# Optimization experiments

Measured on AMD Instinct MI355X. Metric: run time of the kernel, lower is better.

Reference implementation:

```python
import jax, jax.numpy as jnp
import numpy as np

N = 1024      # num_nodes
U = 64        # num_units
IN_DIM = 2    # input feature dim per node
B = 32        # batch
F = IN_DIM + U  # 66, input_size inside _gconv


def _xavier(k, shape):
    fan_in, fan_out = shape[-2], shape[-1]
    std = (2.0 / (fan_in + fan_out)) ** 0.5
    return jax.random.normal(k, shape, jnp.float32) * std


def setup_inputs() -> dict:
    key = jax.random.key(0)
    ks = jax.random.split(key, 14)
    return {
        "inputs": jax.random.normal(ks[0], (B, N * IN_DIM), jnp.float32),
        "hx": jax.random.normal(ks[1], (B, N * U), jnp.float32),
        "adj": jax.random.uniform(ks[2], (2, N, N), jnp.float32),
        "mask": jax.random.uniform(ks[3], (8, N, N), jnp.float32),
        # gate gconv params (output_size = 2U). Note: torch LayerParams caches by
        # shape, so weights_s/weights_i/weights_bp are ONE shared weight, ditto atts/atti.
        "W_ru": _xavier(ks[4], (F, 2 * U)),
        "Watt_ru": _xavier(ks[5], (N, 2 * U, 2 * U)),
        "Watt1_ru": _xavier(ks[6], (N, 2 * U, 1)),
        "Wout_ru": _xavier(ks[7], (6 * U, 2 * U)),
        "b_ru": jnp.ones((2 * U,), jnp.float32),   # bias_start=1.0
        # candidate gconv params (output_size = U)
        "W_c": _xavier(ks[8], (F, U)),
        "Watt_c": _xavier(ks[9], (N, U, U)),
        "Watt1_c": _xavier(ks[10], (N, U, 1)),
        "Wout_c": _xavier(ks[11], (3 * U, U)),
        "b_c": jnp.zeros((U,), jnp.float32),
    }


def _gconv(inputs, state, adj, mask, W, Watt, Watt1, Wout, b):
    Bs = inputs.shape[0]
    x = jnp.concatenate([inputs.reshape(Bs, N, -1), state.reshape(Bs, N, -1)], axis=2)  # [B,N,F]
    Ff = x.shape[2]
    x0 = x.transpose(1, 2, 0).reshape(N, Ff * Bs)  # [N, F*B]
    a0, a1 = adj[0], adj[1]
    # supports in the exact order of the torch loop:
    # adj0, mask0..3*adj0, mask4..7*adj1, adj1  -> 10 matrices
    mats = jnp.concatenate(
        [a0[None], mask[:4] * a0[None], mask[4:] * a1[None], a1[None]], axis=0
    )  # [10,N,N]
    xk = jnp.einsum('mij,jf->mif', mats, x0)  # [10,N,F*B]
    x_all = jnp.concatenate([x0[None], xk], axis=0).reshape(11, N, Ff, Bs)
    x_bp = x_all[0].transpose(2, 0, 1)        # [B,N,F]
    x_i = x_all[1:6].transpose(3, 1, 0, 2)    # [B,N,5,F]
    x_s = x_all[6:].transpose(3, 1, 0, 2)     # [B,N,5,F]
    x_i_p = x_i @ W        # [B,N,5,O] (shared weight, see LayerParams shape cache)
    x_s_p = x_s @ W        # [B,N,5,O]
    x_bp_p = x_bp @ W      # [B,N,O]

    def attend(xp):
        h = jax.nn.relu(jnp.einsum('bnko,noq->bnkq', xp, Watt))     # per-node weights
        s = jnp.einsum('bnkq,nqo->bnko', h, Watt1)[..., 0]          # [B,N,5]
        a = jax.nn.softmax(s, axis=-1)                              # over 5 supports
        return jnp.einsum('bnk,bnko->bno', a, xp)                   # [B,N,O]

    xi = attend(x_i_p)
    xs = attend(x_s_p)
    out = jnp.concatenate([xi, xs, x_bp_p], axis=-1) @ Wout + b     # [B,N,O]
    return out.reshape(Bs, -1)


def reference(inputs, hx, adj, mask, W_ru, Watt_ru, Watt1_ru, Wout_ru, b_ru,
              W_c, Watt_c, Watt1_c, Wout_c, b_c):
    value = jax.nn.sigmoid(_gconv(inputs, hx, adj, mask, W_ru, Watt_ru, Watt1_ru, Wout_ru, b_ru))
    value = value.reshape(-1, N, 2 * U)
    r = value[..., :U].reshape(-1, N * U)
    u = value[..., U:].reshape(-1, N * U)
    c = jnp.tanh(_gconv(inputs, r * hx, adj, mask, W_c, Watt_c, Watt1_c, Wout_c, b_c))
    return u * hx + (1.0 - u) * c
```

## Files before the change

kernel.cpp:

```cpp
#include <hip/hip_runtime.h>
#include <hip/hip_fp16.h>
#include <cstdint>
#include <cstddef>

#define NN 1024
#define BB 32

typedef _Float16 f16x8 __attribute__((ext_vector_type(8)));
typedef _Float16 f16x4 __attribute__((ext_vector_type(4)));
typedef float f32x4 __attribute__((ext_vector_type(4)));

__device__ __forceinline__ void load_lds16(const void* g, void* l) {
  __builtin_amdgcn_global_load_lds(
      (const __attribute__((address_space(1))) void*)g,
      (__attribute__((address_space(3))) void*)l, 16, 0, 0);
}

__global__ __launch_bounds__(256) void k_build_amats(
    const float* __restrict__ adj, const float* __restrict__ mask,
    _Float16* __restrict__ A) {
  int q = blockIdx.x * 256 + threadIdx.x;
  int i = q >> 8;
  int j0 = (q & 255) << 2;
  size_t off = (size_t)i * 1024 + j0;
  float4 a0 = *(const float4*)(adj + off);
  float4 a1 = *(const float4*)(adj + (1u << 20) + off);
  f16x4 r;
  r[0] = a0.x; r[1] = a0.y; r[2] = a0.z; r[3] = a0.w;
  *(f16x4*)(A + off) = r;
  r[0] = a1.x; r[1] = a1.y; r[2] = a1.z; r[3] = a1.w;
  *(f16x4*)(A + (size_t)9 * 1048576 + off) = r;
#pragma unroll
  for (int l = 0; l < 8; ++l) {
    float4 mk = *(const float4*)(mask + (size_t)l * 1048576 + off);
    float4 base = (l < 4) ? a0 : a1;
    r[0] = mk.x * base.x; r[1] = mk.y * base.y;
    r[2] = mk.z * base.z; r[3] = mk.w * base.w;
    *(f16x4*)(A + (size_t)(l + 1) * 1048576 + off) = r;
  }
}

__global__ __launch_bounds__(256) void k_prep_wout(
    const float* __restrict__ Wru, const float* __restrict__ Wc,
    _Float16* __restrict__ WThru, _Float16* __restrict__ WTlru,
    _Float16* __restrict__ WThc, _Float16* __restrict__ WTlc) {
  int id = blockIdx.x * 256 + threadIdx.x;
  if (id < 128 * 384) {
    int o = id & 127, k = id >> 7;
    float w = Wru[k * 128 + o];
    _Float16 h = (_Float16)w;
    WThru[o * 384 + k] = h;
    WTlru[o * 384 + k] = (_Float16)(w - (float)h);
  } else {
    int id2 = id - 128 * 384;
    if (id2 < 64 * 192) {
      int o = id2 & 63, k = id2 >> 6;
      float w = Wc[k * 64 + o];
      _Float16 h = (_Float16)w;
      WThc[o * 192 + k] = h;
      WTlc[o * 192 + k] = (_Float16)(w - (float)h);
    }
  }
}

__global__ __launch_bounds__(256) void k_build_x0p(
    const float* __restrict__ inp, const float* __restrict__ state,
    _Float16* __restrict__ X0P) {
  const int b = blockIdx.x;
  const int j0 = blockIdx.y * 64;
  const int tid = threadIdx.x;
  for (int p = tid; p < 4096; p += 256) {
    int jj = p >> 6, f = p & 63;
    X0P[((size_t)(b * 1024 + j0 + jj)) * 96 + 2 + f] =
        (_Float16)state[(size_t)b * 65536 + (j0 + jj) * 64 + f];
  }
  if (tid < 128) {
    int jj = tid >> 1, f = tid & 1;
    X0P[((size_t)(b * 1024 + j0 + jj)) * 96 + f] =
        (_Float16)inp[(size_t)b * 2048 + (j0 + jj) * 2 + f];
    X0P[((size_t)(b * 1024 + j0 + 32 + jj)) * 96 + f] =
        (_Float16)inp[(size_t)b * 2048 + (j0 + 32 + jj) * 2 + f];
  }
  for (int p = tid; p < 64 * 32; p += 256) {
    int jj = p >> 5, f = 66 + (p & 31);
    if (f < 96)
      X0P[((size_t)(b * 1024 + j0 + jj)) * 96 + f] = (_Float16)0.f;
  }
}

template <int O>
__global__ __launch_bounds__(256, 2) void k_proj0_mfma(
    const _Float16* __restrict__ X0P, const float* __restrict__ W,
    _Float16* __restrict__ XP0, _Float16* __restrict__ XP0T) {
  constexpr int WR = O / 64;
  constexpr int WC = 4 / WR;
  constexpr int TN = WC * 64;
  constexpr int NPT = TN / 64;
  __shared__ _Float16 ldsB[2][TN * 32];
  const int tid = threadIdx.x;
  const int c0 = blockIdx.x * TN;
  const int b = c0 >> 10;
  const int l = tid & 63;
  const int w = tid >> 6;
  const int wr = w / WC, wc = w % WC;

  f16x8 af[4][3];
#pragma unroll
  for (int i = 0; i < 4; ++i) {
    int o = wr * 64 + i * 16 + (l & 15);
#pragma unroll
    for (int ks = 0; ks < 3; ++ks) {
#pragma unroll
      for (int e = 0; e < 8; ++e) {
        int f = ks * 32 + (l >> 4) * 8 + e;
        af[i][ks][e] = (f < 66) ? (_Float16)W[f * O + o] : (_Float16)0.f;
      }
    }
  }

  int tt[NPT], rr[NPT], qq[NPT];
#pragma unroll
  for (int u = 0; u < NPT; ++u) {
    tt[u] = u * 256 + tid;
    rr[u] = tt[u] >> 2;
    qq[u] = (tt[u] & 3) ^ (rr[u] & 3);
  }

  const int ps = ((l >> 4) ^ (l & 3)) * 8;
  int offB[4];
#pragma unroll
  for (int j = 0; j < 4; ++j)
    offB[j] = (wc * 64 + j * 16 + (l & 15)) * 32 + ps;

  f32x4 acc[4][4];
#pragma unroll
  for (int i = 0; i < 4; ++i)
#pragma unroll
    for (int j = 0; j < 4; ++j) acc[i][j] = (f32x4){0.f, 0.f, 0.f, 0.f};

#pragma unroll
  for (int u = 0; u < NPT; ++u)
    load_lds16(X0P + (size_t)(c0 + rr[u]) * 96 + qq[u] * 8,
               &ldsB[0][0] + tt[u] * 8);

  int buf = 0;
  for (int kt = 0; kt < 3; ++kt) {
    __syncthreads();
    if (kt + 1 < 3) {
#pragma unroll
      for (int u = 0; u < NPT; ++u)
        load_lds16(X0P + (size_t)(c0 + rr[u]) * 96 + (kt + 1) * 32 + qq[u] * 8,
                   &ldsB[buf ^ 1][0] + tt[u] * 8);
    }
    f16x8 bf[4];
#pragma unroll
    for (int j = 0; j < 4; ++j) bf[j] = *(const f16x8*)(&ldsB[buf][offB[j]]);
#pragma unroll
    for (int i = 0; i < 4; ++i)
#pragma unroll
      for (int j = 0; j < 4; ++j)
        acc[i][j] = __builtin_amdgcn_mfma_f32_16x16x32_f16(af[i][kt], bf[j],
                                                           acc[i][j], 0, 0, 0);
    buf ^= 1;
  }

#pragma unroll
  for (int i = 0; i < 4; ++i) {
    int ob = wr * 64 + i * 16 + (l >> 4) * 4;
#pragma unroll
    for (int j = 0; j < 4; ++j) {
      int jn = (c0 & 1023) + wc * 64 + j * 16 + (l & 15);
      f16x4 hv;
#pragma unroll
      for (int r = 0; r < 4; ++r) {
        hv[r] = (_Float16)acc[i][j][r];
        XP0T[((size_t)b * O + ob + r) * 1024 + jn] = hv[r];
      }
      *(f16x4*)(XP0 + ((size_t)jn * 32 + b) * O + ob) = hv;
    }
  }
}

template <int CN>
__global__ __launch_bounds__(256, 2) void k_supports2_mfma(
    const _Float16* __restrict__ A, const _Float16* __restrict__ BT,
    _Float16* __restrict__ XPD) {
  __shared__ _Float16 ldsA[2][4096];
  __shared__ _Float16 ldsB[2][4096];
  const int tid = threadIdx.x;
  const int bn = blockIdx.x;
  const int bm = blockIdx.y;
  const int l = tid & 63;
  const int w = tid >> 6;
  const int wr = w >> 1, wc = w & 1;

  const int t0 = tid, t1 = 256 + tid;
  const int r0 = t0 >> 2, q0 = (t0 & 3) ^ (r0 & 3);
  const int r1 = t1 >> 2, q1 = (t1 & 3) ^ (r1 & 3);
  const _Float16* gA0 = A + ((size_t)(bm * 128 + r0)) * 1024 + q0 * 8;
  const _Float16* gA1 = A + ((size_t)(bm * 128 + r1)) * 1024 + q1 * 8;
  const _Float16* gB0 = BT + ((size_t)(bn * 128 + r0)) * 1024 + q0 * 8;
  const _Float16* gB1 = BT + ((size_t)(bn * 128 + r1)) * 1024 + q1 * 8;

  const int ps = ((l >> 4) ^ (l & 3)) * 8;
  int offA[4], offB[4];
#pragma unroll
  for (int i = 0; i < 4; ++i) {
    offA[i] = (wr * 64 + i * 16 + (l & 15)) * 32 + ps;
    offB[i] = (wc * 64 + i * 16 + (l & 15)) * 32 + ps;
  }

  f32x4 acc[4][4];
#pragma unroll
  for (int i = 0; i < 4; ++i)
#pragma unroll
    for (int j = 0; j < 4; ++j) acc[i][j] = (f32x4){0.f, 0.f, 0.f, 0.f};

  load_lds16(gA0, &ldsA[0][0] + t0 * 8);
  load_lds16(gA1, &ldsA[0][0] + t1 * 8);
  load_lds16(gB0, &ldsB[0][0] + t0 * 8);
  load_lds16(gB1, &ldsB[0][0] + t1 * 8);

  int buf = 0;
  for (int kt = 0; kt < 32; ++kt) {
    __syncthreads();
    if (kt + 1 < 32) {
      int k0 = (kt + 1) * 32;
      load_lds16(gA0 + k0, &ldsA[buf ^ 1][0] + t0 * 8);
      load_lds16(gA1 + k0, &ldsA[buf ^ 1][0] + t1 * 8);
      load_lds16(gB0 + k0, &ldsB[buf ^ 1][0] + t0 * 8);
      load_lds16(gB1 + k0, &ldsB[buf ^ 1][0] + t1 * 8);
    }
    f16x8 af[4], bf[4];
#pragma unroll
    for (int i = 0; i < 4; ++i)
      af[i] = *(const f16x8*)(&ldsA[buf][offA[i]]);
#pragma unroll
    for (int i = 0; i < 4; ++i)
      bf[i] = *(const f16x8*)(&ldsB[buf][offB[i]]);
#pragma unroll
    for (int i = 0; i < 4; ++i)
#pragma unroll
      for (int j = 0; j < 4; ++j)
        acc[i][j] = __builtin_amdgcn_mfma_f32_16x16x32_f16(af[i], bf[j],
                                                           acc[i][j], 0, 0, 0);
    buf ^= 1;
  }

#pragma unroll
  for (int i = 0; i < 4; ++i) {
    int R = bm * 128 + wr * 64 + i * 16 + (l >> 4) * 4;
#pragma unroll
    for (int j = 0; j < 4; ++j) {
      int col = bn * 128 + wc * 64 + j * 16 + (l & 15);
#pragma unroll
      for (int r = 0; r < 4; ++r)
        XPD[(size_t)(R + r) * CN + col] = (_Float16)acc[i][j][r];
    }
  }
}

template <int O>
__global__ __launch_bounds__(256) void k_attend_mfma(
    const __half* __restrict__ XPD, const float* __restrict__ Watt,
    const float* __restrict__ Watt1, _Float16* __restrict__ CAT2h,
    _Float16* __restrict__ CAT2l) {
  constexpr int MTW = O / 64;
  constexpr int KS = O / 32;
  constexpr int SLOTS = O / 8;
  constexpr int SWZ = SLOTS - 1;
  constexpr int OH = O / 2;
  const int n = blockIdx.x;
  const int tid = threadIdx.x;
  const int l = tid & 63;
  const int w = tid >> 6;

  __shared__ _Float16 xpL[160 * O];
  __shared__ float sPartL[4][160];
  __shared__ float aL[32][5];

  const int qbase = w * (O / 4);
  f16x8 afr[MTW][KS];
#pragma unroll
  for (int mt = 0; mt < MTW; ++mt) {
    const int q = qbase + mt * 16 + (l & 15);
#pragma unroll
    for (int ks = 0; ks < KS; ++ks) {
#pragma unroll
      for (int e = 0; e < 8; ++e) {
        int o = ks * 32 + (l >> 4) * 8 + e;
        afr[mt][ks][e] = (_Float16)Watt[((size_t)n * O + o) * O + q];
      }
    }
  }
  float wt1[MTW][4];
#pragma unroll
  for (int mt = 0; mt < MTW; ++mt)
#pragma unroll
    for (int r = 0; r < 4; ++r)
      wt1[mt][r] = Watt1[(size_t)n * O + qbase + mt * 16 + (l >> 4) * 4 + r];

  for (int g = 0; g < 2; ++g) {
    if (g) __syncthreads();
    {
      const uint32_t* xsrc = reinterpret_cast<const uint32_t*>(XPD);
      uint32_t* xdst = reinterpret_cast<uint32_t*>(xpL);
      for (int p = tid; p < 160 * OH; p += 256) {
        int row = p / OH;
        int oh = p - row * OH;
        int slot = oh >> 2;
        int phys = slot ^ (row & SWZ);
        int si = row >> 5, b = row & 31;
        size_t gi = ((size_t)(g * 5 + si) * 1024 + n) * (size_t)(16 * O) +
                    b * OH + oh;
        xdst[row * OH + phys * 4 + (oh & 3)] = xsrc[gi];
      }
    }
    __syncthreads();

    for (int nt = 0; nt < 10; ++nt) {
      f32x4 acc[MTW];
#pragma unroll
      for (int mt = 0; mt < MTW; ++mt) acc[mt] = (f32x4){0.f, 0.f, 0.f, 0.f};
      const int row = nt * 16 + (l & 15);
#pragma unroll
      for (int ks = 0; ks < KS; ++ks) {
        int phys = (ks * 4 + (l >> 4)) ^ (row & SWZ);
        f16x8 bf = *(const f16x8*)(&xpL[row * O + phys * 8]);
#pragma unroll
        for (int mt = 0; mt < MTW; ++mt)
          acc[mt] = __builtin_amdgcn_mfma_f32_16x16x32_f16(afr[mt][ks], bf,
                                                           acc[mt], 0, 0, 0);
      }
      float sp = 0.f;
#pragma unroll
      for (int mt = 0; mt < MTW; ++mt)
#pragma unroll
        for (int r = 0; r < 4; ++r)
          sp += fmaxf(acc[mt][r], 0.f) * wt1[mt][r];
      sp += __shfl_xor(sp, 16);
      sp += __shfl_xor(sp, 32);
      if (l < 16) sPartL[w][nt * 16 + l] = sp;
    }
    __syncthreads();

    if (tid < 32) {
      const int b = tid;
      float sv[5];
#pragma unroll
      for (int k = 0; k < 5; ++k) {
        int row = k * 32 + b;
        sv[k] = sPartL[0][row] + sPartL[1][row] + sPartL[2][row] +
                sPartL[3][row];
      }
      float mx = sv[0];
#pragma unroll
      for (int k = 1; k < 5; ++k) mx = fmaxf(mx, sv[k]);
      float e[5], sum = 0.f;
#pragma unroll
      for (int k = 0; k < 5; ++k) {
        e[k] = expf(sv[k] - mx);
        sum += e[k];
      }
      float inv = 1.f / sum;
#pragma unroll
      for (int k = 0; k < 5; ++k) aL[b][k] = e[k] * inv;
    }
    __syncthreads();

    for (int it = 0; it < SLOTS * 32 / 256; ++it) {
      int idx = it * 256 + tid;
      int b = idx & 31;
      int sc = idx >> 5;
      float o8[8] = {0.f, 0.f, 0.f, 0.f, 0.f, 0.f, 0.f, 0.f};
#pragma unroll
      for (int si = 0; si < 5; ++si) {
        int row = si * 32 + b;
        int phys = sc ^ (row & SWZ);
        f16x8 xv = *(const f16x8*)(&xpL[row * O + phys * 8]);
        float a = aL[b][si];
#pragma unroll
        for (int j = 0; j < 8; ++j) o8[j] += a * (float)xv[j];
      }
      f16x8 hv, lv;
#pragma unroll
      for (int j = 0; j < 8; ++j) {
        hv[j] = (_Float16)o8[j];
        lv[j] = (_Float16)(o8[j] - (float)hv[j]);
      }
      size_t doff = ((size_t)n * 32 + b) * (2 * O) + g * O + sc * 8;
      *reinterpret_cast<f16x8*>(CAT2h + doff) = hv;
      *reinterpret_cast<f16x8*>(CAT2l + doff) = lv;
    }
  }
}

__global__ __launch_bounds__(256, 2) void k_wout_ru_mfma(
    const _Float16* __restrict__ CAT2h, const _Float16* __restrict__ CAT2l,
    const _Float16* __restrict__ XP0, const _Float16* __restrict__ WTh,
    const _Float16* __restrict__ WTl, const float* __restrict__ bias,
    const float* __restrict__ hx, float* __restrict__ RHX,
    float* __restrict__ UBUF) {
  constexpr int KTOT = 384, KC = 8, KT = 12;
  __shared__ _Float16 ldsAh[2][4096];
  __shared__ _Float16 ldsAl[2][4096];
  __shared__ _Float16 ldsBh[2][4096];
  __shared__ _Float16 ldsBl[2][4096];
  const int tid = threadIdx.x;
  const int blk = blockIdx.x;
  const int l = tid & 63;
  const int w = tid >> 6;
  const int wr = w >> 1, wc = w & 1;

  const int t0 = tid, t1 = 256 + tid;
  const int r0 = t0 >> 2, q0 = (t0 & 3) ^ (r0 & 3);
  const int r1 = t1 >> 2, q1 = (t1 & 3) ^ (r1 & 3);
  const size_t R0 = (size_t)blk * 128 + r0, R1 = (size_t)blk * 128 + r1;
  const _Float16* pA0ch = CAT2h + R0 * 256 + q0 * 8;
  const _Float16* pA1ch = CAT2h + R1 * 256 + q1 * 8;
  const _Float16* pA0cl = CAT2l + R0 * 256 + q0 * 8;
  const _Float16* pA1cl = CAT2l + R1 * 256 + q1 * 8;
  const _Float16* pA0x = XP0 + R0 * 128 + q0 * 8;
  const _Float16* pA1x = XP0 + R1 * 128 + q1 * 8;
  const _Float16* pB0h = WTh + (size_t)r0 * KTOT + q0 * 8;
  const _Float16* pB1h = WTh + (size_t)r1 * KTOT + q1 * 8;
  const _Float16* pB0l = WTl + (size_t)r0 * KTOT + q0 * 8;
  const _Float16* pB1l = WTl + (size_t)r1 * KTOT + q1 * 8;

  const int ps = ((l >> 4) ^ (l & 3)) * 8;
  int offA[4], offB[4];
#pragma unroll
  for (int i = 0; i < 4; ++i) {
    offA[i] = (wr * 64 + i * 16 + (l & 15)) * 32 + ps;
    offB[i] = (wc * 64 + i * 16 + (l & 15)) * 32 + ps;
  }

  f32x4 acc[4][4];
#pragma unroll
  for (int i = 0; i < 4; ++i)
#pragma unroll
    for (int j = 0; j < 4; ++j) acc[i][j] = (f32x4){0.f, 0.f, 0.f, 0.f};

  load_lds16(pA0ch, &ldsAh[0][0] + t0 * 8);
  load_lds16(pA1ch, &ldsAh[0][0] + t1 * 8);
  load_lds16(pA0cl, &ldsAl[0][0] + t0 * 8);
  load_lds16(pA1cl, &ldsAl[0][0] + t1 * 8);
  load_lds16(pB0h, &ldsBh[0][0] + t0 * 8);
  load_lds16(pB1h, &ldsBh[0][0] + t1 * 8);
  load_lds16(pB0l, &ldsBl[0][0] + t0 * 8);
  load_lds16(pB1l, &ldsBl[0][0] + t1 * 8);

  int buf = 0;
  for (int kt = 0; kt < KT; ++kt) {
    __syncthreads();
    if (kt + 1 < KT) {
      int k1 = kt + 1;
      const _Float16* a0 =
          (k1 < KC) ? pA0ch + k1 * 32 : pA0x + (k1 - KC) * 32;
      const _Float16* a1 =
          (k1 < KC) ? pA1ch + k1 * 32 : pA1x + (k1 - KC) * 32;
      load_lds16(a0, &ldsAh[buf ^ 1][0] + t0 * 8);
      load_lds16(a1, &ldsAh[buf ^ 1][0] + t1 * 8);
      if (k1 < KC) {
        load_lds16(pA0cl + k1 * 32, &ldsAl[buf ^ 1][0] + t0 * 8);
        load_lds16(pA1cl + k1 * 32, &ldsAl[buf ^ 1][0] + t1 * 8);
      }
      load_lds16(pB0h + k1 * 32, &ldsBh[buf ^ 1][0] + t0 * 8);
      load_lds16(pB1h + k1 * 32, &ldsBh[buf ^ 1][0] + t1 * 8);
      load_lds16(pB0l + k1 * 32, &ldsBl[buf ^ 1][0] + t0 * 8);
      load_lds16(pB1l + k1 * 32, &ldsBl[buf ^ 1][0] + t1 * 8);
    }
    f16x8 ah[4], bh[4], bl[4];
#pragma unroll
    for (int i = 0; i < 4; ++i) ah[i] = *(const f16x8*)(&ldsAh[buf][offA[i]]);
#pragma unroll
    for (int i = 0; i < 4; ++i) bh[i] = *(const f16x8*)(&ldsBh[buf][offB[i]]);
#pragma unroll
    for (int i = 0; i < 4; ++i) bl[i] = *(const f16x8*)(&ldsBl[buf][offB[i]]);
#pragma unroll
    for (int i = 0; i < 4; ++i)
#pragma unroll
      for (int j = 0; j < 4; ++j) {
        acc[i][j] = __builtin_amdgcn_mfma_f32_16x16x32_f16(ah[i], bh[j],
                                                           acc[i][j], 0, 0, 0);
        acc[i][j] = __builtin_amdgcn_mfma_f32_16x16x32_f16(ah[i], bl[j],
                                                           acc[i][j], 0, 0, 0);
      }
    if (kt < KC) {
      f16x8 al[4];
#pragma unroll
      for (int i = 0; i < 4; ++i)
        al[i] = *(const f16x8*)(&ldsAl[buf][offA[i]]);
#pragma unroll
      for (int i = 0; i < 4; ++i)
#pragma unroll
        for (int j = 0; j < 4; ++j)
          acc[i][j] = __builtin_amdgcn_mfma_f32_16x16x32_f16(al[i], bh[j],
                                                             acc[i][j], 0, 0, 0);
    }
    buf ^= 1;
  }

#pragma unroll
  for (int i = 0; i < 4; ++i) {
    int R = blk * 128 + wr * 64 + i * 16 + (l >> 4) * 4;
#pragma unroll
    for (int j = 0; j < 4; ++j) {
      int o = wc * 64 + j * 16 + (l & 15);
      float bv = bias[o];
#pragma unroll
      for (int rr = 0; rr < 4; ++rr) {
        int Rr = R + rr;
        int n = Rr >> 5, b = Rr & 31;
        size_t base = ((size_t)b * NN + n) * 64;
        float val = 1.f / (1.f + expf(-(acc[i][j][rr] + bv)));
        if (o < 64)
          RHX[base + o] = val * hx[base + o];
        else
          UBUF[base + (o - 64)] = val;
      }
    }
  }
}

__global__ __launch_bounds__(256, 2) void k_wout_c_mfma(
    const _Float16* __restrict__ CAT2h, const _Float16* __restrict__ CAT2l,
    const _Float16* __restrict__ XP0, const _Float16* __restrict__ WTh,
    const _Float16* __restrict__ WTl, const float* __restrict__ bias,
    const float* __restrict__ UBUF, const float* __restrict__ hx,
    float* __restrict__ out) {
  constexpr int KTOT = 192, KC = 4, KT = 6;
  __shared__ _Float16 ldsAh[2][4096];
  __shared__ _Float16 ldsAl[2][4096];
  __shared__ _Float16 ldsBh[2][2048];
  __shared__ _Float16 ldsBl[2][2048];
  const int tid = threadIdx.x;
  const int blk = blockIdx.x;
  const int l = tid & 63;
  const int w = tid >> 6;

  const int t0 = tid, t1 = 256 + tid;
  const int r0 = t0 >> 2, q0 = (t0 & 3) ^ (r0 & 3);
  const int r1 = t1 >> 2, q1 = (t1 & 3) ^ (r1 & 3);
  const size_t R0 = (size_t)blk * 128 + r0, R1 = (size_t)blk * 128 + r1;
  const _Float16* pA0ch = CAT2h + R0 * 128 + q0 * 8;
  const _Float16* pA1ch = CAT2h + R1 * 128 + q1 * 8;
  const _Float16* pA0cl = CAT2l + R0 * 128 + q0 * 8;
  const _Float16* pA1cl = CAT2l + R1 * 128 + q1 * 8;
  const _Float16* pA0x = XP0 + R0 * 64 + q0 * 8;
  const _Float16* pA1x = XP0 + R1 * 64 + q1 * 8;
  const int rb = tid >> 2, qb = (tid & 3) ^ (rb & 3);
  const _Float16* pBh = WTh + (size_t)rb * KTOT + qb * 8;
  const _Float16* pBl = WTl + (size_t)rb * KTOT + qb * 8;

  const int ps = ((l >> 4) ^ (l & 3)) * 8;
  int offA[2], offB[4];
#pragma unroll
  for (int i = 0; i < 2; ++i)
    offA[i] = (w * 32 + i * 16 + (l & 15)) * 32 + ps;
#pragma unroll
  for (int j = 0; j < 4; ++j) offB[j] = (j * 16 + (l & 15)) * 32 + ps;

  f32x4 acc[2][4];
#pragma unroll
  for (int i = 0; i < 2; ++i)
#pragma unroll
    for (int j = 0; j < 4; ++j) acc[i][j] = (f32x4){0.f, 0.f, 0.f, 0.f};

  load_lds16(pA0ch, &ldsAh[0][0] + t0 * 8);
  load_lds16(pA1ch, &ldsAh[0][0] + t1 * 8);
  load_lds16(pA0cl, &ldsAl[0][0] + t0 * 8);
  load_lds16(pA1cl, &ldsAl[0][0] + t1 * 8);
  load_lds16(pBh, &ldsBh[0][0] + tid * 8);
  load_lds16(pBl, &ldsBl[0][0] + tid * 8);

  int buf = 0;
  for (int kt = 0; kt < KT; ++kt) {
    __syncthreads();
    if (kt + 1 < KT) {
      int k1 = kt + 1;
      const _Float16* a0 =
          (k1 < KC) ? pA0ch + k1 * 32 : pA0x + (k1 - KC) * 32;
      const _Float16* a1 =
          (k1 < KC) ? pA1ch + k1 * 32 : pA1x + (k1 - KC) * 32;
      load_lds16(a0, &ldsAh[buf ^ 1][0] + t0 * 8);
      load_lds16(a1, &ldsAh[buf ^ 1][0] + t1 * 8);
      if (k1 < KC) {
        load_lds16(pA0cl + k1 * 32, &ldsAl[buf ^ 1][0] + t0 * 8);
        load_lds16(pA1cl + k1 * 32, &ldsAl[buf ^ 1][0] + t1 * 8);
      }
      load_lds16(pBh + k1 * 32, &ldsBh[buf ^ 1][0] + tid * 8);
      load_lds16(pBl + k1 * 32, &ldsBl[buf ^ 1][0] + tid * 8);
    }
    f16x8 ah[2], bh[4], bl[4];
#pragma unroll
    for (int i = 0; i < 2; ++i) ah[i] = *(const f16x8*)(&ldsAh[buf][offA[i]]);
#pragma unroll
    for (int j = 0; j < 4; ++j) bh[j] = *(const f16x8*)(&ldsBh[buf][offB[j]]);
#pragma unroll
    for (int j = 0; j < 4; ++j) bl[j] = *(const f16x8*)(&ldsBl[buf][offB[j]]);
#pragma unroll
    for (int i = 0; i < 2; ++i)
#pragma unroll
      for (int j = 0; j < 4; ++j) {
        acc[i][j] = __builtin_amdgcn_mfma_f32_16x16x32_f16(ah[i], bh[j],
                                                           acc[i][j], 0, 0, 0);
        acc[i][j] = __builtin_amdgcn_mfma_f32_16x16x32_f16(ah[i], bl[j],
                                                           acc[i][j], 0, 0, 0);
      }
    if (kt < KC) {
      f16x8 al[2];
#pragma unroll
      for (int i = 0; i < 2; ++i)
        al[i] = *(const f16x8*)(&ldsAl[buf][offA[i]]);
#pragma unroll
      for (int i = 0; i < 2; ++i)
#pragma unroll
        for (int j = 0; j < 4; ++j)
          acc[i][j] = __builtin_amdgcn_mfma_f32_16x16x32_f16(al[i], bh[j],
                                                             acc[i][j], 0, 0, 0);
    }
    buf ^= 1;
  }

#pragma unroll
  for (int i = 0; i < 2; ++i) {
    int R = blk * 128 + w * 32 + i * 16 + (l >> 4) * 4;
#pragma unroll
    for (int j = 0; j < 4; ++j) {
      int o = j * 16 + (l & 15);
      float bv = bias[o];
#pragma unroll
      for (int rr = 0; rr < 4; ++rr) {
        int Rr = R + rr;
        int n = Rr >> 5, b = Rr & 31;
        size_t idx = ((size_t)b * NN + n) * 64 + o;
        float cval = tanhf(acc[i][j][rr] + bv);
        float u = UBUF[idx];
        out[idx] = u * hx[idx] + (1.f - u) * cval;
      }
    }
  }
}

extern "C" void kernel_launch(void* const* d_in, const int* in_sizes, int n_in,
                              void* d_out, int out_size, void* d_ws,
                              size_t ws_size, hipStream_t stream) {
  const float* inputs   = (const float*)d_in[0];
  const float* hx       = (const float*)d_in[1];
  const float* adj      = (const float*)d_in[2];
  const float* mask     = (const float*)d_in[3];
  const float* W_ru     = (const float*)d_in[4];
  const float* Watt_ru  = (const float*)d_in[5];
  const float* Watt1_ru = (const float*)d_in[6];
  const float* Wout_ru  = (const float*)d_in[7];
  const float* b_ru     = (const float*)d_in[8];
  const float* W_c      = (const float*)d_in[9];
  const float* Watt_c   = (const float*)d_in[10];
  const float* Watt1_c  = (const float*)d_in[11];
  const float* Wout_c   = (const float*)d_in[12];
  const float* b_c      = (const float*)d_in[13];

  char* ws = (char*)d_ws;
  _Float16*  X0P   = (_Float16*)(ws);
  _Float16*  XPD   = (_Float16*)(ws + 6291456);
  _Float16*  XP0   = (_Float16*)(ws + 90177536);
  _Float16*  XP0T  = (_Float16*)(ws + 98566144);
  _Float16*  CAT2h = (_Float16*)(ws + 106954752);
  _Float16*  CAT2l = (_Float16*)(ws + 123731968);
  float*     RHX   = (float*)(ws + 140509184);
  float*     UBUF  = (float*)(ws + 148897792);
  _Float16*  A_all = (_Float16*)(ws + 157286400);
  _Float16*  WThru = (_Float16*)(ws + 178257920);
  _Float16*  WTlru = (_Float16*)(ws + 178356224);
  _Float16*  WThc  = (_Float16*)(ws + 178454528);
  _Float16*  WTlc  = (_Float16*)(ws + 178479104);
  float*     out   = (float*)d_out;

  k_build_amats<<<1024, 256, 0, stream>>>(adj, mask, A_all);
  k_prep_wout<<<240, 256, 0, stream>>>(Wout_ru, Wout_c, WThru, WTlru, WThc,
                                       WTlc);

  k_build_x0p<<<dim3(32, 16), 256, 0, stream>>>(inputs, hx, X0P);
  k_proj0_mfma<128><<<256, 256, 0, stream>>>(X0P, W_ru, XP0, XP0T);
  k_supports2_mfma<4096><<<dim3(32, 80), 256, 0, stream>>>(A_all, XP0T, XPD);
  k_attend_mfma<128><<<1024, 256, 0, stream>>>((const __half*)XPD, Watt_ru,
                                               Watt1_ru, CAT2h, CAT2l);
  k_wout_ru_mfma<<<256, 256, 0, stream>>>(CAT2h, CAT2l, XP0, WThru, WTlru,
                                          b_ru, hx, RHX, UBUF);
  k_build_x0p<<<dim3(32, 16), 256, 0, stream>>>(inputs, RHX, X0P);
  k_proj0_mfma<64><<<128, 256, 0, stream>>>(X0P, W_c, XP0, XP0T);
  k_supports2_mfma<2048><<<dim3(16, 80), 256, 0, stream>>>(A_all, XP0T, XPD);
  k_attend_mfma<64><<<1024, 256, 0, stream>>>((const __half*)XPD, Watt_c,
                                              Watt1_c, CAT2h, CAT2l);
  k_wout_c_mfma<<<256, 256, 0, stream>>>(CAT2h, CAT2l, XP0, WThc, WTlc, b_c,
                                         UBUF, hx, out);
}
```

Baseline: 344.5 us.

## Use 32x32 MFMA and XCD-aware block swizzle in supports GEMM; drop split-fp16 in wout_c

The supports GEMM switches from 16x16x32 MFMA tiles to 32x32x16 MFMA tiles. Fewer LDS fragment reads and MFMA issues are needed per K step. Workgroups are remapped so consecutive blocks on each XCD share A/B tiles in L2. Separately, the candidate Wout GEMM drops the low-order fp16 correction terms (hi/lo split), which removes extra loads and MFMAs at the cost of reduced precision in the final output.

Measured after the change: 374.6 us. 1.09x slower.

```diff
diff --git a/kernel.cpp b/kernel.cpp
--- a/kernel.cpp
+++ b/kernel.cpp
@@ -9,6 +9,7 @@
 typedef _Float16 f16x8 __attribute__((ext_vector_type(8)));
 typedef _Float16 f16x4 __attribute__((ext_vector_type(4)));
 typedef float f32x4 __attribute__((ext_vector_type(4)));
+typedef float f32x16 __attribute__((ext_vector_type(16)));
 
 __device__ __forceinline__ void load_lds16(const void* g, void* l) {
   __builtin_amdgcn_global_load_lds(
@@ -188,8 +189,13 @@
   __shared__ _Float16 ldsA[2][4096];
   __shared__ _Float16 ldsB[2][4096];
   const int tid = threadIdx.x;
-  const int bn = blockIdx.x;
-  const int bm = blockIdx.y;
+  constexpr int GX = CN / 128;
+  const int flat = blockIdx.x + GX * blockIdx.y;
+  constexpr int NWG = GX * 80;
+  constexpr int CPX = NWG / 8;
+  const int swz = (flat & 7) * CPX + (flat >> 3);
+  const int bn = swz % GX;
+  const int bm = swz / GX;
   const int l = tid & 63;
   const int w = tid >> 6;
   const int wr = w >> 1, wc = w & 1;
@@ -202,19 +208,23 @@
   const _Float16* gB0 = BT + ((size_t)(bn * 128 + r0)) * 1024 + q0 * 8;
   const _Float16* gB1 = BT + ((size_t)(bn * 128 + r1)) * 1024 + q1 * 8;
 
-  const int ps = ((l >> 4) ^ (l & 3)) * 8;
-  int offA[4], offB[4];
-#pragma unroll
-  for (int i = 0; i < 4; ++i) {
-    offA[i] = (wr * 64 + i * 16 + (l & 15)) * 32 + ps;
-    offB[i] = (wc * 64 + i * 16 + (l & 15)) * 32 + ps;
-  }
-
-  f32x4 acc[4][4];
-#pragma unroll
-  for (int i = 0; i < 4; ++i)
-#pragma unroll
-    for (int j = 0; j < 4; ++j) acc[i][j] = (f32x4){0.f, 0.f, 0.f, 0.f};
+  int offA[2][2], offB[2][2];
+#pragma unroll
+  for (int fi = 0; fi < 2; ++fi)
+#pragma unroll
+    for (int ks = 0; ks < 2; ++ks) {
+      int slot = ((ks * 2 + (l >> 5)) ^ (l & 3)) * 8;
+      offA[fi][ks] = (wr * 64 + fi * 32 + (l & 31)) * 32 + slot;
+      offB[fi][ks] = (wc * 64 + fi * 32 + (l & 31)) * 32 + slot;
+    }
+
+  f32x16 acc[2][2];
+#pragma unroll
+  for (int i = 0; i < 2; ++i)
+#pragma unroll
+    for (int j = 0; j < 2; ++j)
+#pragma unroll
+      for (int e = 0; e < 16; ++e) acc[i][j][e] = 0.f;
 
   load_lds16(gA0, &ldsA[0][0] + t0 * 8);
   load_lds16(gA1, &ldsA[0][0] + t1 * 8);
@@ -231,33 +241,37 @@
       load_lds16(gB0 + k0, &ldsB[buf ^ 1][0] + t0 * 8);
       load_lds16(gB1 + k0, &ldsB[buf ^ 1][0] + t1 * 8);
     }
-    f16x8 af[4], bf[4];
-#pragma unroll
-    for (int i = 0; i < 4; ++i)
-      af[i] = *(const f16x8*)(&ldsA[buf][offA[i]]);
-#pragma unroll
-    for (int i = 0; i < 4; ++i)
-      bf[i] = *(const f16x8*)(&ldsB[buf][offB[i]]);
-#pragma unroll
-    for (int i = 0; i < 4; ++i)
-#pragma unroll
-      for (int j = 0; j < 4; ++j)
-        acc[i][j] = __builtin_amdgcn_mfma_f32_16x16x32_f16(af[i], bf[j],
-                                                           acc[i][j], 0, 0, 0);
+    f16x8 af[2][2], bf[2][2];
+#pragma unroll
+    for (int fi = 0; fi < 2; ++fi)
+#pragma unroll
+      for (int ks = 0; ks < 2; ++ks) {
+        af[fi][ks] = *(const f16x8*)(&ldsA[buf][offA[fi][ks]]);
+        bf[fi][ks] = *(const f16x8*)(&ldsB[buf][offB[fi][ks]]);
+      }
+#pragma unroll
+    for (int fi = 0; fi < 2; ++fi)
+#pragma unroll
+      for (int fj = 0; fj < 2; ++fj)
+#pragma unroll
+        for (int ks = 0; ks < 2; ++ks)
+          acc[fi][fj] = __builtin_amdgcn_mfma_f32_32x32x16_f16(
+              af[fi][ks], bf[fj][ks], acc[fi][fj], 0, 0, 0);
     buf ^= 1;
   }
 
 #pragma unroll
-  for (int i = 0; i < 4; ++i) {
-    int R = bm * 128 + wr * 64 + i * 16 + (l >> 4) * 4;
-#pragma unroll
-    for (int j = 0; j < 4; ++j) {
-      int col = bn * 128 + wc * 64 + j * 16 + (l & 15);
-#pragma unroll
-      for (int r = 0; r < 4; ++r)
-        XPD[(size_t)(R + r) * CN + col] = (_Float16)acc[i][j][r];
-    }
-  }
+  for (int fi = 0; fi < 2; ++fi)
+#pragma unroll
+    for (int fj = 0; fj < 2; ++fj) {
+      int colg = bn * 128 + wc * 64 + fj * 32 + (l & 31);
+      int Rb = bm * 128 + wr * 64 + fi * 32 + 4 * (l >> 5);
+#pragma unroll
+      for (int e = 0; e < 16; ++e) {
+        int R = Rb + (e & 3) + 8 * (e >> 2);
+        XPD[(size_t)R * CN + colg] = (_Float16)acc[fi][fj][e];
+      }
+    }
 }
 
 template <int O>
@@ -524,16 +538,13 @@
 }
 
 __global__ __launch_bounds__(256, 2) void k_wout_c_mfma(
-    const _Float16* __restrict__ CAT2h, const _Float16* __restrict__ CAT2l,
-    const _Float16* __restrict__ XP0, const _Float16* __restrict__ WTh,
-    const _Float16* __restrict__ WTl, const float* __restrict__ bias,
+    const _Float16* __restrict__ CAT2h, const _Float16* __restrict__ XP0,
+    const _Float16* __restrict__ WTh, const float* __restrict__ bias,
     const float* __restrict__ UBUF, const float* __restrict__ hx,
     float* __restrict__ out) {
   constexpr int KTOT = 192, KC = 4, KT = 6;
   __shared__ _Float16 ldsAh[2][4096];
-  __shared__ _Float16 ldsAl[2][4096];
   __shared__ _Float16 ldsBh[2][2048];
-  __shared__ _Float16 ldsBl[2][2048];
   const int tid = threadIdx.x;
   const int blk = blockIdx.x;
   const int l = tid & 63;
@@ -545,13 +556,10 @@
   const size_t R0 = (size_t)blk * 128 + r0, R1 = (size_t)blk * 128 + r1;
   const _Float16* pA0ch = CAT2h + R0 * 128 + q0 * 8;
   const _Float16* pA1ch = CAT2h + R1 * 128 + q1 * 8;
-  const _Float16* pA0cl = CAT2l + R0 * 128 + q0 * 8;
-  const _Float16* pA1cl = CAT2l + R1 * 128 + q1 * 8;
   const _Float16* pA0x = XP0 + R0 * 64 + q0 * 8;
   const _Float16* pA1x = XP0 + R1 * 64 + q1 * 8;
   const int rb = tid >> 2, qb = (tid & 3) ^ (rb & 3);
   const _Float16* pBh = WTh + (size_t)rb * KTOT + qb * 8;
-  const _Float16* pBl = WTl + (size_t)rb * KTOT + qb * 8;
 
   const int ps = ((l >> 4) ^ (l & 3)) * 8;
   int offA[2], offB[4];
@@ -569,10 +577,7 @@
 
   load_lds16(pA0ch, &ldsAh[0][0] + t0 * 8);
   load_lds16(pA1ch, &ldsAh[0][0] + t1 * 8);
-  load_lds16(pA0cl, &ldsAl[0][0] + t0 * 8);
-  load_lds16(pA1cl, &ldsAl[0][0] + t1 * 8);
   load_lds16(pBh, &ldsBh[0][0] + tid * 8);
-  load_lds16(pBl, &ldsBl[0][0] + tid * 8);
 
   int buf = 0;
   for (int kt = 0; kt < KT; ++kt) {
@@ -585,41 +590,19 @@
           (k1 < KC) ? pA1ch + k1 * 32 : pA1x + (k1 - KC) * 32;
       load_lds16(a0, &ldsAh[buf ^ 1][0] + t0 * 8);
       load_lds16(a1, &ldsAh[buf ^ 1][0] + t1 * 8);
-      if (k1 < KC) {
-        load_lds16(pA0cl + k1 * 32, &ldsAl[buf ^ 1][0] + t0 * 8);
-        load_lds16(pA1cl + k1 * 32, &ldsAl[buf ^ 1][0] + t1 * 8);
-      }
       load_lds16(pBh + k1 * 32, &ldsBh[buf ^ 1][0] + tid * 8);
-      load_lds16(pBl + k1 * 32, &ldsBl[buf ^ 1][0] + tid * 8);
-    }
-    f16x8 ah[2], bh[4], bl[4];
+    }
+    f16x8 ah[2], bh[4];
 #pragma unroll
     for (int i = 0; i < 2; ++i) ah[i] = *(const f16x8*)(&ldsAh[buf][offA[i]]);
 #pragma unroll
     for (int j = 0; j < 4; ++j) bh[j] = *(const f16x8*)(&ldsBh[buf][offB[j]]);
 #pragma unroll
-    for (int j = 0; j < 4; ++j) bl[j] = *(const f16x8*)(&ldsBl[buf][offB[j]]);
-#pragma unroll
     for (int i = 0; i < 2; ++i)
 #pragma unroll
-      for (int j = 0; j < 4; ++j) {
+      for (int j = 0; j < 4; ++j)
         acc[i][j] = __builtin_amdgcn_mfma_f32_16x16x32_f16(ah[i], bh[j],
                                                            acc[i][j], 0, 0, 0);
-        acc[i][j] = __builtin_amdgcn_mfma_f32_16x16x32_f16(ah[i], bl[j],
-                                                           acc[i][j], 0, 0, 0);
-      }
-    if (kt < KC) {
-      f16x8 al[2];
-#pragma unroll
-      for (int i = 0; i < 2; ++i)
-        al[i] = *(const f16x8*)(&ldsAl[buf][offA[i]]);
-#pragma unroll
-      for (int i = 0; i < 2; ++i)
-#pragma unroll
-        for (int j = 0; j < 4; ++j)
-          acc[i][j] = __builtin_amdgcn_mfma_f32_16x16x32_f16(al[i], bh[j],
-                                                             acc[i][j], 0, 0, 0);
-    }
     buf ^= 1;
   }
 
@@ -693,6 +676,6 @@
   k_supports2_mfma<2048><<<dim3(16, 80), 256, 0, stream>>>(A_all, XP0T, XPD);
   k_attend_mfma<64><<<1024, 256, 0, stream>>>((const __half*)XPD, Watt_c,
                                               Watt1_c, CAT2h, CAT2l);
-  k_wout_c_mfma<<<256, 256, 0, stream>>>(CAT2h, CAT2l, XP0, WThc, WTlc, b_c,
+  k_wout_c_mfma<<<256, 256, 0, stream>>>(CAT2h, XP0, WThc, b_c,
                                          UBUF, hx, out);
 }
```
